# Performance work log

Measured on AMD Instinct MI355X. Metric: run time of the kernel, lower is better.

Reference implementation:

```python
import jax, jax.numpy as jnp
import numpy as np

B, S, D, H = 4, 1024, 1024, 16
HD = D // H


def setup_inputs() -> dict:
    key = jax.random.key(0)
    ks = jax.random.split(key, 8)
    x = jax.random.normal(ks[0], (B, S, D), dtype=jnp.float32)
    attn_bias = jax.random.normal(ks[1], (B, H, S, S), dtype=jnp.float32) * 0.1
    pos_ids = jnp.broadcast_to(jnp.arange(S, dtype=jnp.int32), (B, S))
    lengths = jnp.array([S, S - 64, S - 128, S - 256], dtype=jnp.int32)
    pad_mask = jnp.arange(S)[None, :] >= lengths[:, None]  # True = padded key
    scale = 0.02
    Wq = jax.random.normal(ks[2], (D, D), dtype=jnp.float32) * scale
    Wk = jax.random.normal(ks[3], (D, D), dtype=jnp.float32) * scale
    Wv = jax.random.normal(ks[4], (D, D), dtype=jnp.float32) * scale
    Wo = jax.random.normal(ks[5], (D, D), dtype=jnp.float32) * scale
    bq = jnp.zeros((D,), jnp.float32); bk = jnp.zeros((D,), jnp.float32)
    bv = jnp.zeros((D,), jnp.float32); bo = jnp.zeros((D,), jnp.float32)
    return {"x": x, "attn_bias": attn_bias, "pos_ids": pos_ids, "pad_mask": pad_mask,
            "Wq": Wq, "bq": bq, "Wk": Wk, "bk": bk, "Wv": Wv, "bv": bv, "Wo": Wo, "bo": bo}


def _apply_rotary(q, k, pos_ids):
    # q,k: [B,S,H,HD]; pos_ids: [B,S]
    hd = q.shape[-1]
    inv_freq = 1.0 / (10000.0 ** (jnp.arange(0, hd, 2, dtype=jnp.float32) / hd))
    freqs = pos_ids.astype(jnp.float32)[:, :, None] * inv_freq  # [B,S,HD/2]
    emb = jnp.concatenate([freqs, freqs], axis=-1)[:, :, None, :]  # [B,S,1,HD]
    cos, sin = jnp.cos(emb), jnp.sin(emb)
    def rot_half(t):
        t1, t2 = jnp.split(t, 2, axis=-1)
        return jnp.concatenate([-t2, t1], axis=-1)
    return q * cos + rot_half(q) * sin, k * cos + rot_half(k) * sin


def reference(x, attn_bias, pos_ids, pad_mask, Wq, bq, Wk, bk, Wv, bv, Wo, bo):
    b, s, d = x.shape
    q = (x @ Wq.T + bq).reshape(b, s, H, HD)
    k = (x @ Wk.T + bk).reshape(b, s, H, HD)
    v = (x @ Wv.T + bv).reshape(b, s, H, HD)
    q, k = _apply_rotary(q, k, pos_ids)
    q = q.transpose(0, 2, 1, 3)  # [B,H,S,HD]
    k = k.transpose(0, 2, 1, 3)
    v = v.transpose(0, 2, 1, 3)
    scores = jnp.einsum("bhqd,bhkd->bhqk", q, k) / np.sqrt(HD).astype(np.float32)
    scores = scores + attn_bias
    scores = jnp.where(pad_mask[:, None, None, :], -jnp.inf, scores)
    attn = jax.nn.softmax(scores, axis=-1)  # dropout p=0 -> identity
    out = jnp.einsum("bhqk,bhkd->bqhd", attn, v).reshape(b, s, d)
    metric = k.mean(axis=1)  # mean over heads -> [B,S,HD]
    return out @ Wo.T + bo, metric
```

## Files before the change

### kernel.cpp

```cpp
#include <hip/hip_runtime.h>
#include <hip/hip_bf16.h>

#define SS 1024
#define DD 1024
#define HH 16
#define HDD 64

using f32x4  = __attribute__((ext_vector_type(4))) float;
using bf16x8 = __attribute__((ext_vector_type(8))) __bf16;
using bf16x4 = __attribute__((ext_vector_type(4))) __bf16;

__device__ __forceinline__ void gload_lds16(const void* g, void* l) {
  __builtin_amdgcn_global_load_lds((__attribute__((address_space(1))) void*)g,
                                   (__attribute__((address_space(3))) void*)l, 16, 0, 0);
}

__global__ void convert_kernel(const float4* __restrict__ x, const float4* __restrict__ Wq,
                               const float4* __restrict__ Wk, const float4* __restrict__ Wv,
                               const float4* __restrict__ Wo,
                               bf16x4* __restrict__ xb, bf16x4* __restrict__ wqkvb,
                               bf16x4* __restrict__ wob, float4* __restrict__ metric) {
  int i = blockIdx.x * 256 + threadIdx.x;
  if (blockIdx.x < 256) {
    float4 z = {0.f, 0.f, 0.f, 0.f};
    metric[blockIdx.x * 256 + threadIdx.x] = z;
  }
  float4 v; bf16x4* dst;
  if (i < 1048576)      { v = x[i];              dst = xb + i; }
  else if (i < 1310720) { v = Wq[i - 1048576];   dst = wqkvb + (i - 1048576); }
  else if (i < 1572864) { v = Wk[i - 1310720];   dst = wqkvb + 262144 + (i - 1310720); }
  else if (i < 1835008) { v = Wv[i - 1572864];   dst = wqkvb + 524288 + (i - 1572864); }
  else                  { v = Wo[i - 1835008];   dst = wob + (i - 1835008); }
  bf16x4 o;
  o[0] = (__bf16)v.x; o[1] = (__bf16)v.y; o[2] = (__bf16)v.z; o[3] = (__bf16)v.w;
  *dst = o;
}

#define GEMM_STAGE(BUF, KK)                                                        \
  {                                                                                \
    char* Ab = smem + (BUF) * 32768;                                               \
    char* Bb = Ab + 16384;                                                         \
    _Pragma("unroll") for (int q = 0; q < 4; ++q) {                                \
      int idx = q * 256 + tid;                                                     \
      int row = idx >> 3, c = idx & 7;                                             \
      gload_lds16(A  + (size_t)(m0 + row) * 1024 + (KK) + ((c ^ (row & 7)) << 3),  \
                  Ab + q * 4096 + wid * 1024);                                     \
      gload_lds16(Bm + (size_t)(n0 + row) * 1024 + (KK) + ((c ^ (row & 7)) << 3),  \
                  Bb + q * 4096 + wid * 1024);                                     \
    }                                                                              \
  }

template<int EPI>
__global__ __launch_bounds__(256, 2)
void gemm_kernel(const __bf16* __restrict__ A, const __bf16* __restrict__ Bm, int N,
                 const float* __restrict__ b0, const float* __restrict__ b1,
                 const float* __restrict__ b2, const int* __restrict__ pos_ids,
                 __bf16* __restrict__ Qr, __bf16* __restrict__ Kr, __bf16* __restrict__ Vtg,
                 float* __restrict__ metric, float* __restrict__ Cout) {
  __shared__ __align__(16) char smem[65536];
  const int tid = threadIdx.x;
  const int wid = tid >> 6, lane = tid & 63;
  const int g = lane >> 4, cl = lane & 15;
  const int ntn = N >> 7;
  const int tile = (blockIdx.x & 7) * ((int)gridDim.x >> 3) + (blockIdx.x >> 3);
  const int bm = tile / ntn, bn = tile % ntn;
  const int m0 = bm << 7, n0 = bn << 7;
  const int wr = (wid >> 1) << 6, wc = (wid & 1) << 6;
  const int swz = cl & 7;

  f32x4 acc[4][4] = {};

  GEMM_STAGE(0, 0);
  __syncthreads();
  int buf = 0;
  for (int t = 0; t < 16; ++t) {
    if (t + 1 < 16) GEMM_STAGE(buf ^ 1, (t + 1) * 64);
    const __bf16* Abuf = (const __bf16*)(smem + buf * 32768);
    const __bf16* Bbuf = Abuf + 8192;
#pragma unroll
    for (int s = 0; s < 2; ++s) {
      bf16x8 fa[4], fb[4];
#pragma unroll
      for (int i = 0; i < 4; ++i)
        fa[i] = *(const bf16x8*)(Abuf + (wr + i * 16 + cl) * 64 + (((s * 4 + g) ^ swz) << 3));
#pragma unroll
      for (int j = 0; j < 4; ++j)
        fb[j] = *(const bf16x8*)(Bbuf + (wc + j * 16 + cl) * 64 + (((s * 4 + g) ^ swz) << 3));
#pragma unroll
      for (int i = 0; i < 4; ++i)
#pragma unroll
        for (int j = 0; j < 4; ++j)
          acc[i][j] = __builtin_amdgcn_mfma_f32_16x16x32_bf16(fa[i], fb[j], acc[i][j], 0, 0, 0);
    }
    __syncthreads();
    buf ^= 1;
  }

  if constexpr (EPI == 1) {
#pragma unroll
    for (int j = 0; j < 4; ++j) {
      int col = n0 + wc + j * 16 + cl;
      float bv = b0[col];
#pragma unroll
      for (int i = 0; i < 4; ++i)
#pragma unroll
        for (int r = 0; r < 4; ++r) {
          int row = m0 + wr + i * 16 + g * 4 + r;
          Cout[(size_t)row * 1024 + col] = acc[i][j][r] + bv;
        }
    }
  } else if (n0 >= 2048) {
    __bf16* vt_s = (__bf16*)smem;
    const int b_ = m0 >> 10, s0 = m0 & 1023;
    const int vbase = n0 - 2048;
#pragma unroll
    for (int phase = 0; phase < 2; ++phase) {
      __syncthreads();
      if ((wid & 1) == phase) {
#pragma unroll
        for (int j = 0; j < 4; ++j) {
          int d = j * 16 + cl;
          float bv = b2[vbase + wc + d];
#pragma unroll
          for (int i = 0; i < 4; ++i)
#pragma unroll
            for (int r = 0; r < 4; ++r)
              vt_s[d * 136 + wr + i * 16 + g * 4 + r] = (__bf16)(acc[i][j][r] + bv);
        }
      }
      __syncthreads();
      int hh = (vbase >> 6) + phase;
#pragma unroll
      for (int p = 0; p < 4; ++p) {
        int d = p * 16 + (tid >> 4), s8 = (tid & 15) * 8;
        bf16x8 v = *(const bf16x8*)(vt_s + d * 136 + s8);
        *(bf16x8*)(Vtg + ((size_t)(b_ * HH + hh) * HDD + d) * SS + s0 + s8) = v;
      }
    }
  } else {
    const int cb = n0 + wc;
    const int region = cb >> 10;
    const int hcol = (cb & 1023) >> 6;
    const int cir = cb & 1023;
    const float* bias = region == 0 ? b0 : b1;
    __bf16* dst = region == 0 ? Qr : Kr;
    float invf0 = exp2f(-0.4152410118609203f * (float)(cl));
    float invf1 = exp2f(-0.4152410118609203f * (float)(16 + cl));
#pragma unroll
    for (int i = 0; i < 4; ++i) {
#pragma unroll
      for (int r = 0; r < 4; ++r) {
        int row = m0 + wr + i * 16 + g * 4 + r;
        int b_ = row >> 10, s = row & 1023;
        size_t ob = ((size_t)(b_ * HH + hcol) * SS + s) * HDD;
        float pos = (float)pos_ids[row];
#pragma unroll
        for (int j = 0; j < 2; ++j) {
          int dlo = j * 16 + cl;
          float vlo = acc[i][j][r]     + bias[cir + dlo];
          float vhi = acc[i][j + 2][r] + bias[cir + dlo + 32];
          float th = pos * (j == 0 ? invf0 : invf1);
          float sn, cs;
          __sincosf(th, &sn, &cs);
          float olo = vlo * cs - vhi * sn;
          float ohi = vhi * cs + vlo * sn;
          dst[ob + dlo]      = (__bf16)olo;
          dst[ob + dlo + 32] = (__bf16)ohi;
          if (region == 1) {
            atomicAdd(&metric[(size_t)row * HDD + dlo],      olo * 0.0625f);
            atomicAdd(&metric[(size_t)row * HDD + dlo + 32], ohi * 0.0625f);
          }
        }
      }
    }
  }
}

#define ATTN_HALF(KT0, W0, BCUR)                                                   \
  {                                                                                \
    f32x4 sc[4];                                                                   \
    __builtin_amdgcn_s_setprio(1);                                                 \
    _Pragma("unroll") for (int kt = 0; kt < 4; ++kt) {                             \
      int row = (KT0 + kt) * 16 + cl;                                              \
      bf16x8 kb0 = *(const bf16x8*)(&Ks[buf][row][(g ^ swz) * 8]);                 \
      bf16x8 kb1 = *(const bf16x8*)(&Ks[buf][row][((g + 4) ^ swz) * 8]);           \
      f32x4 z = {0.f, 0.f, 0.f, 0.f};                                              \
      z = __builtin_amdgcn_mfma_f32_16x16x32_bf16(kb0, aq0, z, 0, 0, 0);           \
      sc[kt] = __builtin_amdgcn_mfma_f32_16x16x32_bf16(kb1, aq1, z, 0, 0, 0);      \
    }                                                                              \
    __builtin_amdgcn_s_setprio(0);                                                 \
    _Pragma("unroll") for (int kt = 0; kt < 4; ++kt)                               \
      _Pragma("unroll") for (int r = 0; r < 4; ++r)                                \
        sc[kt][r] = sc[kt][r] * 0.125f + BCUR[KT0 + kt][r];                        \
    float mx = fmaxf(fmaxf(fmaxf(sc[0][0], sc[0][1]), fmaxf(sc[0][2], sc[0][3])),  \
                     fmaxf(fmaxf(sc[1][0], sc[1][1]), fmaxf(sc[1][2], sc[1][3]))); \
    mx = fmaxf(mx, fmaxf(fmaxf(fmaxf(sc[2][0], sc[2][1]), fmaxf(sc[2][2], sc[2][3])), \
                         fmaxf(fmaxf(sc[3][0], sc[3][1]), fmaxf(sc[3][2], sc[3][3])))); \
    mx = fmaxf(mx, __shfl_xor(mx, 16, 64));                                        \
    mx = fmaxf(mx, __shfl_xor(mx, 32, 64));                                        \
    if (!__all(mx <= m_l + 8.0f)) {                                                \
      float nm = fmaxf(m_l, mx);                                                   \
      float s_ = __expf(m_l - nm);                                                 \
      m_l = nm; l_l *= s_;                                                         \
      float sb0 = __shfl(s_, 4 * g + 0, 64), sb1 = __shfl(s_, 4 * g + 1, 64);      \
      float sb2 = __shfl(s_, 4 * g + 2, 64), sb3 = __shfl(s_, 4 * g + 3, 64);      \
      _Pragma("unroll") for (int dj = 0; dj < 4; ++dj) {                           \
        o[dj][0] *= sb0; o[dj][1] *= sb1; o[dj][2] *= sb2; o[dj][3] *= sb3;        \
      }                                                                            \
    }                                                                              \
    _Pragma("unroll") for (int kt = 0; kt < 4; ++kt)                               \
      _Pragma("unroll") for (int r = 0; r < 4; ++r)                                \
        sc[kt][r] = __expf(sc[kt][r] - m_l);                                       \
    float rs = ((sc[0][0] + sc[0][1]) + (sc[0][2] + sc[0][3]))                     \
             + ((sc[1][0] + sc[1][1]) + (sc[1][2] + sc[1][3]))                     \
             + ((sc[2][0] + sc[2][1]) + (sc[2][2] + sc[2][3]))                     \
             + ((sc[3][0] + sc[3][1]) + (sc[3][2] + sc[3][3]));                    \
    rs += __shfl_xor(rs, 16, 64);                                                  \
    rs += __shfl_xor(rs, 32, 64);                                                  \
    l_l += rs;                                                                     \
    _Pragma("unroll") for (int w = 0; w < 2; ++w) {                                \
      _Pragma("unroll") for (int k2 = 0; k2 < 2; ++k2) {                           \
        int kt = w * 2 + k2;                                                       \
        bf16x4 pk;                                                                 \
        pk[0] = (__bf16)sc[kt][0]; pk[1] = (__bf16)sc[kt][1];                      \
        pk[2] = (__bf16)sc[kt][2]; pk[3] = (__bf16)sc[kt][3];                      \
        *(bf16x4*)(Pw + cl * 40 + k2 * 16 + 4 * g) = pk;                           \
      }                                                                            \
      bf16x8 pa = *(const bf16x8*)(Pw + cl * 40 + g * 8);                          \
      __builtin_amdgcn_s_setprio(1);                                               \
      _Pragma("unroll") for (int dj = 0; dj < 4; ++dj) {                           \
        int vrow = dj * 16 + cl;                                                   \
        bf16x8 vb = *(const bf16x8*)(&Vt[buf][vrow][((((W0 + w) * 4) + g) ^ swz) * 8]); \
        o[dj] = __builtin_amdgcn_mfma_f32_16x16x32_bf16(pa, vb, o[dj], 0, 0, 0);   \
      }                                                                            \
      __builtin_amdgcn_s_setprio(0);                                               \
    }                                                                              \
  }

#define ATTN_STAGE(NB, KK)                                                         \
  _Pragma("unroll") for (int s = 0; s < 2; ++s) {                                  \
    gload_lds16(Kb + (size_t)((KK) + s * 64 + krow) * 64 + kchk * 8,               \
                (char*)&Ks[NB][s * 64 + 8 * wid][0]);                              \
    gload_lds16(Vb + (size_t)(s * 32 + vrow) * SS + (KK) + vchk * 8,               \
                (char*)&Vt[NB][s * 32 + 4 * wid][0]);                              \
  }

__global__ __launch_bounds__(512, 4)
void attn_kernel(const __bf16* __restrict__ Qr, const __bf16* __restrict__ Kr,
                 const __bf16* __restrict__ Vtg, const float* __restrict__ bias,
                 const int* __restrict__ pad, __bf16* __restrict__ attn_out) {
  __shared__ __align__(16) __bf16 Ks[2][128][64];
  __shared__ __align__(16) __bf16 Vt[2][64][128];
  __shared__ __align__(16) __bf16 Plds[8][16][40];
  const int tid = threadIdx.x;
  const int wid = tid >> 6, lane = tid & 63;
  const int g = lane >> 4, cl = lane & 15;
  const int bh = blockIdx.x & 63, b_ = bh >> 4, h = bh & 15;
  const int q0 = (blockIdx.x >> 6) * 128 + wid * 16;
  const __bf16* Qb = Qr  + ((size_t)bh << 16);
  const __bf16* Kb = Kr  + ((size_t)bh << 16);
  const __bf16* Vb = Vtg + ((size_t)bh << 16);
  const float*  Bb = bias + ((size_t)bh << 20);
  const int* padb = pad + b_ * SS;

  int pm = (lane < 16) ? padb[lane * 64] : 1;
  unsigned long long ball = __ballot(pm == 0);
  const int valid64 = __popcll(ball & 0xFFFFull);
  const int nt = (valid64 + 1) >> 1;
  const int tail = valid64 & 1;

  const int krow = 8 * wid + (lane >> 3);
  const int kchk = (lane & 7) ^ (lane >> 3);
  const int vrow = 4 * wid + (lane >> 4);
  const int vchk = (lane & 15) ^ (vrow & 7);
  const int swz = cl & 7;
  __bf16* Pw = &Plds[wid][0][0];

  bf16x8 aq0 = *(const bf16x8*)(Qb + (size_t)(q0 + cl) * 64 + g * 8);
  bf16x8 aq1 = *(const bf16x8*)(Qb + (size_t)(q0 + cl) * 64 + 32 + g * 8);
  __builtin_amdgcn_sched_barrier(0);

  ATTN_STAGE(0, 0);
  __builtin_amdgcn_sched_barrier(0);
  f32x4 breg[8];
#pragma unroll
  for (int kt = 0; kt < 8; ++kt)
    breg[kt] = *(const f32x4*)(Bb + (size_t)(q0 + cl) * SS + kt * 16 + 4 * g);
  __builtin_amdgcn_sched_barrier(0);

  f32x4 o[4] = {};
  float m_l = -1e30f, l_l = 0.f;

  for (int t = 0; t < nt; ++t) {
    const int buf = t & 1;
    asm volatile("s_waitcnt vmcnt(8)" ::: "memory");
    __builtin_amdgcn_s_barrier();
    __builtin_amdgcn_sched_barrier(0);
    if (t + 1 < nt) {
      ATTN_STAGE(buf ^ 1, (t + 1) * 128);
      __builtin_amdgcn_sched_barrier(0);
    }

    ATTN_HALF(0, 0, breg);

    if (t + 1 < nt) {
      int kk2 = (t + 1) * 128;
#pragma unroll
      for (int kt = 0; kt < 4; ++kt)
        breg[kt] = *(const f32x4*)(Bb + (size_t)(q0 + cl) * SS + kk2 + kt * 16 + 4 * g);
      __builtin_amdgcn_sched_barrier(0);
    }

    if (!(tail && t == nt - 1))
      ATTN_HALF(4, 2, breg);

    if (t + 1 < nt) {
      int kk2 = (t + 1) * 128;
#pragma unroll
      for (int kt = 4; kt < 8; ++kt)
        breg[kt] = *(const f32x4*)(Bb + (size_t)(q0 + cl) * SS + kk2 + kt * 16 + 4 * g);
      __builtin_amdgcn_sched_barrier(0);
    }
  }

  float lb0 = __shfl(l_l, 4 * g + 0, 64), lb1 = __shfl(l_l, 4 * g + 1, 64);
  float lb2 = __shfl(l_l, 4 * g + 2, 64), lb3 = __shfl(l_l, 4 * g + 3, 64);
  float ib0 = 1.f / lb0, ib1 = 1.f / lb1, ib2 = 1.f / lb2, ib3 = 1.f / lb3;
#pragma unroll
  for (int dj = 0; dj < 4; ++dj) {
    int col = h * 64 + dj * 16 + cl;
    attn_out[(size_t)(b_ * SS + q0 + g * 4 + 0) * DD + col] = (__bf16)(o[dj][0] * ib0);
    attn_out[(size_t)(b_ * SS + q0 + g * 4 + 1) * DD + col] = (__bf16)(o[dj][1] * ib1);
    attn_out[(size_t)(b_ * SS + q0 + g * 4 + 2) * DD + col] = (__bf16)(o[dj][2] * ib2);
    attn_out[(size_t)(b_ * SS + q0 + g * 4 + 3) * DD + col] = (__bf16)(o[dj][3] * ib3);
  }
}

extern "C" void kernel_launch(void* const* d_in, const int* in_sizes, int n_in,
                              void* d_out, int out_size, void* d_ws, size_t ws_size,
                              hipStream_t stream) {
  const float* x  = (const float*)d_in[0];
  const float* ab = (const float*)d_in[1];
  const int* pos  = (const int*)d_in[2];
  const int* pad  = (const int*)d_in[3];
  const float* Wq = (const float*)d_in[4];
  const float* bq = (const float*)d_in[5];
  const float* Wk = (const float*)d_in[6];
  const float* bk = (const float*)d_in[7];
  const float* Wv = (const float*)d_in[8];
  const float* bv = (const float*)d_in[9];
  const float* Wo = (const float*)d_in[10];
  const float* bo = (const float*)d_in[11];
  float* out = (float*)d_out;
  float* metric = out + 4194304;

  char* ws = (char*)d_ws;
  __bf16* Qr   = (__bf16*)(ws);
  __bf16* Kr   = (__bf16*)(ws + 8388608);
  __bf16* Vtg  = (__bf16*)(ws + 16777216);
  __bf16* xb   = (__bf16*)(ws + 25165824);
  __bf16* wqkv = (__bf16*)(ws + 33554432);
  __bf16* wob  = (__bf16*)(ws + 39845888);
  __bf16* ao   = (__bf16*)(ws + 41943040);

  convert_kernel<<<8192, 256, 0, stream>>>((const float4*)x, (const float4*)Wq,
                                           (const float4*)Wk, (const float4*)Wv,
                                           (const float4*)Wo, (bf16x4*)xb,
                                           (bf16x4*)wqkv, (bf16x4*)wob, (float4*)metric);
  gemm_kernel<0><<<768, 256, 0, stream>>>(xb, wqkv, 3072, bq, bk, bv, pos,
                                          Qr, Kr, Vtg, metric, nullptr);
  attn_kernel<<<512, 512, 0, stream>>>(Qr, Kr, Vtg, ab, pad, ao);
  gemm_kernel<1><<<256, 256, 0, stream>>>(ao, wob, 1024, bo, nullptr, nullptr, nullptr,
                                          nullptr, nullptr, nullptr, nullptr, out);
}
```

Measured before the change: 155.3 us.

## Use 256x256 tiles with 8 waves for the QKV projection GEMM

The QKV projection GEMM moves from 128x128 tiles with 4 waves to 256x256 tiles with 8 waves, using 128KB of dynamic shared memory for double buffering. Prefetch loads are interleaved with the MFMA quarters, and priority and scheduling barriers are added. The larger tile is meant to raise arithmetic intensity and cut global and LDS traffic per FLOP. The cost is only 192 blocks on a GPU with 256 CUs, at one block per CU, so some CUs sit idle and there is less latency hiding. The output-projection GEMM is split out unchanged as its own kernel.

```diff
diff --git a/kernel.cpp b/kernel.cpp
--- a/kernel.cpp
+++ b/kernel.cpp
@@ -36,109 +36,120 @@
   *dst = o;
 }
 
-#define GEMM_STAGE(BUF, KK)                                                        \
-  {                                                                                \
-    char* Ab = smem + (BUF) * 32768;                                               \
-    char* Bb = Ab + 16384;                                                         \
-    _Pragma("unroll") for (int q = 0; q < 4; ++q) {                                \
-      int idx = q * 256 + tid;                                                     \
-      int row = idx >> 3, c = idx & 7;                                             \
-      gload_lds16(A  + (size_t)(m0 + row) * 1024 + (KK) + ((c ^ (row & 7)) << 3),  \
-                  Ab + q * 4096 + wid * 1024);                                     \
-      gload_lds16(Bm + (size_t)(n0 + row) * 1024 + (KK) + ((c ^ (row & 7)) << 3),  \
-                  Bb + q * 4096 + wid * 1024);                                     \
-    }                                                                              \
-  }
-
-template<int EPI>
-__global__ __launch_bounds__(256, 2)
-void gemm_kernel(const __bf16* __restrict__ A, const __bf16* __restrict__ Bm, int N,
+__global__ __launch_bounds__(512, 2)
+void gemm256_qkv(const __bf16* __restrict__ A, const __bf16* __restrict__ Bm,
                  const float* __restrict__ b0, const float* __restrict__ b1,
                  const float* __restrict__ b2, const int* __restrict__ pos_ids,
                  __bf16* __restrict__ Qr, __bf16* __restrict__ Kr, __bf16* __restrict__ Vtg,
-                 float* __restrict__ metric, float* __restrict__ Cout) {
-  __shared__ __align__(16) char smem[65536];
+                 float* __restrict__ metric) {
+  extern __shared__ __align__(16) char smem[];
   const int tid = threadIdx.x;
   const int wid = tid >> 6, lane = tid & 63;
   const int g = lane >> 4, cl = lane & 15;
-  const int ntn = N >> 7;
-  const int tile = (blockIdx.x & 7) * ((int)gridDim.x >> 3) + (blockIdx.x >> 3);
-  const int bm = tile / ntn, bn = tile % ntn;
-  const int m0 = bm << 7, n0 = bn << 7;
-  const int wr = (wid >> 1) << 6, wc = (wid & 1) << 6;
+  const int tile = (blockIdx.x & 7) * 24 + (blockIdx.x >> 3);
+  const int bm = tile / 12, bn = tile % 12;
+  const int m0 = bm << 8, n0 = bn << 8;
+  const int wm = wid >> 2, wn = wid & 3;
+  const int wr = wm << 7, wc = wn << 6;
   const int swz = cl & 7;
 
-  f32x4 acc[4][4] = {};
-
-  GEMM_STAGE(0, 0);
+  f32x4 acc[8][4] = {};
+
+  const int srow = tid >> 3, schk0 = tid & 7;
+
+#define G256_STAGE_ONE(DSTBASE, SRC, Q, KK)                                        \
+  {                                                                                \
+    int row_ = (Q) * 64 + srow;                                                    \
+    gload_lds16(SRC + (size_t)(row_) * 1024 + (KK) + ((schk0 ^ (row_ & 7)) << 3),  \
+                (char*)(DSTBASE) + (Q) * 8192 + wid * 1024);                       \
+  }
+
+  {
+    char* Ab = smem;  char* Bb = smem + 32768;
+#pragma unroll
+    for (int q = 0; q < 4; ++q) {
+      G256_STAGE_ONE(Ab, (A + (size_t)m0 * 1024), q, 0);
+      G256_STAGE_ONE(Bb, (Bm + (size_t)n0 * 1024), q, 0);
+    }
+  }
   __syncthreads();
-  int buf = 0;
+
   for (int t = 0; t < 16; ++t) {
-    if (t + 1 < 16) GEMM_STAGE(buf ^ 1, (t + 1) * 64);
-    const __bf16* Abuf = (const __bf16*)(smem + buf * 32768);
-    const __bf16* Bbuf = Abuf + 8192;
-#pragma unroll
-    for (int s = 0; s < 2; ++s) {
-      bf16x8 fa[4], fb[4];
+    const __bf16* As = (const __bf16*)(smem + (t & 1) * 65536);
+    const __bf16* Bs = As + 16384;
+    char* Adst = smem + ((t + 1) & 1) * 65536;
+    char* Bdst = Adst + 32768;
+    const int kk1 = (t + 1) * 64;
+    const bool pf = (t + 1 < 16);
+
+#pragma unroll
+    for (int p = 0; p < 4; ++p) {
+      if (pf) {
+        G256_STAGE_ONE(Adst, (A + (size_t)m0 * 1024), p, kk1);
+        G256_STAGE_ONE(Bdst, (Bm + (size_t)n0 * 1024), p, kk1);
+      }
+      const int qm = p & 1, qn = p >> 1;
+      bf16x8 fa0[4], fa1[4], fb0[2], fb1[2];
+#pragma unroll
+      for (int i = 0; i < 4; ++i) {
+        const __bf16* rp = As + (size_t)(wr + qm * 64 + i * 16 + cl) * 64;
+        fa0[i] = *(const bf16x8*)(rp + ((g ^ swz) << 3));
+        fa1[i] = *(const bf16x8*)(rp + (((4 + g) ^ swz) << 3));
+      }
+#pragma unroll
+      for (int j = 0; j < 2; ++j) {
+        const __bf16* rp = Bs + (size_t)(wc + qn * 32 + j * 16 + cl) * 64;
+        fb0[j] = *(const bf16x8*)(rp + ((g ^ swz) << 3));
+        fb1[j] = *(const bf16x8*)(rp + (((4 + g) ^ swz) << 3));
+      }
+      __builtin_amdgcn_s_setprio(1);
 #pragma unroll
       for (int i = 0; i < 4; ++i)
-        fa[i] = *(const bf16x8*)(Abuf + (wr + i * 16 + cl) * 64 + (((s * 4 + g) ^ swz) << 3));
-#pragma unroll
-      for (int j = 0; j < 4; ++j)
-        fb[j] = *(const bf16x8*)(Bbuf + (wc + j * 16 + cl) * 64 + (((s * 4 + g) ^ swz) << 3));
-#pragma unroll
-      for (int i = 0; i < 4; ++i)
-#pragma unroll
-        for (int j = 0; j < 4; ++j)
-          acc[i][j] = __builtin_amdgcn_mfma_f32_16x16x32_bf16(fa[i], fb[j], acc[i][j], 0, 0, 0);
+#pragma unroll
+        for (int j = 0; j < 2; ++j) {
+          acc[qm * 4 + i][qn * 2 + j] = __builtin_amdgcn_mfma_f32_16x16x32_bf16(
+              fa0[i], fb0[j], acc[qm * 4 + i][qn * 2 + j], 0, 0, 0);
+          acc[qm * 4 + i][qn * 2 + j] = __builtin_amdgcn_mfma_f32_16x16x32_bf16(
+              fa1[i], fb1[j], acc[qm * 4 + i][qn * 2 + j], 0, 0, 0);
+        }
+      __builtin_amdgcn_s_setprio(0);
+      __builtin_amdgcn_sched_barrier(0);
     }
     __syncthreads();
-    buf ^= 1;
-  }
-
-  if constexpr (EPI == 1) {
-#pragma unroll
-    for (int j = 0; j < 4; ++j) {
-      int col = n0 + wc + j * 16 + cl;
-      float bv = b0[col];
-#pragma unroll
-      for (int i = 0; i < 4; ++i)
-#pragma unroll
-        for (int r = 0; r < 4; ++r) {
-          int row = m0 + wr + i * 16 + g * 4 + r;
-          Cout[(size_t)row * 1024 + col] = acc[i][j][r] + bv;
-        }
-    }
-  } else if (n0 >= 2048) {
+  }
+
+  const int cb = n0 + wc;
+  if (cb >= 2048) {
     __bf16* vt_s = (__bf16*)smem;
     const int b_ = m0 >> 10, s0 = m0 & 1023;
     const int vbase = n0 - 2048;
-#pragma unroll
-    for (int phase = 0; phase < 2; ++phase) {
-      __syncthreads();
-      if ((wid & 1) == phase) {
+    __syncthreads();
+#pragma unroll
+    for (int hl = 0; hl < 4; ++hl) {
+      if (wn == hl) {
 #pragma unroll
         for (int j = 0; j < 4; ++j) {
           int d = j * 16 + cl;
-          float bv = b2[vbase + wc + d];
-#pragma unroll
-          for (int i = 0; i < 4; ++i)
+          float bv = b2[vbase + hl * 64 + d];
+#pragma unroll
+          for (int i = 0; i < 8; ++i)
 #pragma unroll
             for (int r = 0; r < 4; ++r)
-              vt_s[d * 136 + wr + i * 16 + g * 4 + r] = (__bf16)(acc[i][j][r] + bv);
+              vt_s[d * 264 + wr + i * 16 + g * 4 + r] = (__bf16)(acc[i][j][r] + bv);
         }
       }
       __syncthreads();
-      int hh = (vbase >> 6) + phase;
+      int hh = (vbase >> 6) + hl;
 #pragma unroll
       for (int p = 0; p < 4; ++p) {
-        int d = p * 16 + (tid >> 4), s8 = (tid & 15) * 8;
-        bf16x8 v = *(const bf16x8*)(vt_s + d * 136 + s8);
+        int idx = p * 512 + tid;
+        int d = idx >> 5, s8 = (idx & 31) * 8;
+        bf16x8 v = *(const bf16x8*)(vt_s + d * 264 + s8);
         *(bf16x8*)(Vtg + ((size_t)(b_ * HH + hh) * HDD + d) * SS + s0 + s8) = v;
       }
+      __syncthreads();
     }
   } else {
-    const int cb = n0 + wc;
     const int region = cb >> 10;
     const int hcol = (cb & 1023) >> 6;
     const int cir = cb & 1023;
@@ -147,7 +158,7 @@
     float invf0 = exp2f(-0.4152410118609203f * (float)(cl));
     float invf1 = exp2f(-0.4152410118609203f * (float)(16 + cl));
 #pragma unroll
-    for (int i = 0; i < 4; ++i) {
+    for (int i = 0; i < 8; ++i) {
 #pragma unroll
       for (int r = 0; r < 4; ++r) {
         int row = m0 + wr + i * 16 + g * 4 + r;
@@ -173,6 +184,75 @@
         }
       }
     }
+  }
+}
+
+#define GEMM_STAGE(BUF, KK)                                                        \
+  {                                                                                \
+    char* Ab = smem + (BUF) * 32768;                                               \
+    char* Bb = Ab + 16384;                                                         \
+    _Pragma("unroll") for (int q = 0; q < 4; ++q) {                                \
+      int idx = q * 256 + tid;                                                     \
+      int row = idx >> 3, c = idx & 7;                                             \
+      gload_lds16(A  + (size_t)(m0 + row) * 1024 + (KK) + ((c ^ (row & 7)) << 3),  \
+                  Ab + q * 4096 + wid * 1024);                                     \
+      gload_lds16(Bm + (size_t)(n0 + row) * 1024 + (KK) + ((c ^ (row & 7)) << 3),  \
+                  Bb + q * 4096 + wid * 1024);                                     \
+    }                                                                              \
+  }
+
+__global__ __launch_bounds__(256, 2)
+void gemm_oproj(const __bf16* __restrict__ A, const __bf16* __restrict__ Bm,
+                const float* __restrict__ b0, float* __restrict__ Cout) {
+  __shared__ __align__(16) char smem[65536];
+  const int tid = threadIdx.x;
+  const int wid = tid >> 6, lane = tid & 63;
+  const int g = lane >> 4, cl = lane & 15;
+  const int tile = (blockIdx.x & 7) * ((int)gridDim.x >> 3) + (blockIdx.x >> 3);
+  const int bm = tile >> 3, bn = tile & 7;
+  const int m0 = bm << 7, n0 = bn << 7;
+  const int wr = (wid >> 1) << 6, wc = (wid & 1) << 6;
+  const int swz = cl & 7;
+
+  f32x4 acc[4][4] = {};
+
+  GEMM_STAGE(0, 0);
+  __syncthreads();
+  int buf = 0;
+  for (int t = 0; t < 16; ++t) {
+    if (t + 1 < 16) GEMM_STAGE(buf ^ 1, (t + 1) * 64);
+    const __bf16* Abuf = (const __bf16*)(smem + buf * 32768);
+    const __bf16* Bbuf = Abuf + 8192;
+#pragma unroll
+    for (int s = 0; s < 2; ++s) {
+      bf16x8 fa[4], fb[4];
+#pragma unroll
+      for (int i = 0; i < 4; ++i)
+        fa[i] = *(const bf16x8*)(Abuf + (wr + i * 16 + cl) * 64 + (((s * 4 + g) ^ swz) << 3));
+#pragma unroll
+      for (int j = 0; j < 4; ++j)
+        fb[j] = *(const bf16x8*)(Bbuf + (wc + j * 16 + cl) * 64 + (((s * 4 + g) ^ swz) << 3));
+#pragma unroll
+      for (int i = 0; i < 4; ++i)
+#pragma unroll
+        for (int j = 0; j < 4; ++j)
+          acc[i][j] = __builtin_amdgcn_mfma_f32_16x16x32_bf16(fa[i], fb[j], acc[i][j], 0, 0, 0);
+    }
+    __syncthreads();
+    buf ^= 1;
+  }
+
+#pragma unroll
+  for (int j = 0; j < 4; ++j) {
+    int col = n0 + wc + j * 16 + cl;
+    float bv = b0[col];
+#pragma unroll
+    for (int i = 0; i < 4; ++i)
+#pragma unroll
+      for (int r = 0; r < 4; ++r) {
+        int row = m0 + wr + i * 16 + g * 4 + r;
+        Cout[(size_t)row * 1024 + col] = acc[i][j][r] + bv;
+      }
   }
 }
 
@@ -363,13 +443,15 @@
   __bf16* wob  = (__bf16*)(ws + 39845888);
   __bf16* ao   = (__bf16*)(ws + 41943040);
 
+  hipFuncSetAttribute((const void*)gemm256_qkv,
+                      hipFuncAttributeMaxDynamicSharedMemorySize, 131072);
+
   convert_kernel<<<8192, 256, 0, stream>>>((const float4*)x, (const float4*)Wq,
                                            (const float4*)Wk, (const float4*)Wv,
                                            (const float4*)Wo, (bf16x4*)xb,
                                            (bf16x4*)wqkv, (bf16x4*)wob, (float4*)metric);
-  gemm_kernel<0><<<768, 256, 0, stream>>>(xb, wqkv, 3072, bq, bk, bv, pos,
-                                          Qr, Kr, Vtg, metric, nullptr);
+  gemm256_qkv<<<192, 512, 131072, stream>>>(xb, wqkv, bq, bk, bv, pos,
+                                            Qr, Kr, Vtg, metric);
   attn_kernel<<<512, 512, 0, stream>>>(Qr, Kr, Vtg, ab, pad, ao);
-  gemm_kernel<1><<<256, 256, 0, stream>>>(ao, wob, 1024, bo, nullptr, nullptr, nullptr,
-                                          nullptr, nullptr, nullptr, nullptr, out);
-}
+  gemm_oproj<<<256, 256, 0, stream>>>(ao, wob, bo, out);
+}
```

After: 158.7 us. 2.2% more time.

## Compute head-mean metric via averaged K weights instead of atomics

Applied to the files above, without the earlier changes.

Uses linearity (rotary is identical across heads) to precompute the head-averaged K weight rows and bias in a new prep kernel. These are appended as an extra 128-wide N tile to the QKV GEMM, whose epilogue writes the metric directly. This removes the metric zeroing and the per-element atomicAdds in the K epilogue. The cost is one extra small kernel and 32 more GEMM tiles, which are half-wasted since only the first 64 columns are used. Precision also changes because averaged weights are rounded to bf16.

```diff
diff --git a/kernel.cpp b/kernel.cpp
--- a/kernel.cpp
+++ b/kernel.cpp
@@ -19,12 +19,8 @@
                                const float4* __restrict__ Wk, const float4* __restrict__ Wv,
                                const float4* __restrict__ Wo,
                                bf16x4* __restrict__ xb, bf16x4* __restrict__ wqkvb,
-                               bf16x4* __restrict__ wob, float4* __restrict__ metric) {
+                               bf16x4* __restrict__ wob) {
   int i = blockIdx.x * 256 + threadIdx.x;
-  if (blockIdx.x < 256) {
-    float4 z = {0.f, 0.f, 0.f, 0.f};
-    metric[blockIdx.x * 256 + threadIdx.x] = z;
-  }
   float4 v; bf16x4* dst;
   if (i < 1048576)      { v = x[i];              dst = xb + i; }
   else if (i < 1310720) { v = Wq[i - 1048576];   dst = wqkvb + (i - 1048576); }
@@ -34,6 +30,29 @@
   bf16x4 o;
   o[0] = (__bf16)v.x; o[1] = (__bf16)v.y; o[2] = (__bf16)v.z; o[3] = (__bf16)v.w;
   *dst = o;
+}
+
+__global__ void prep_kernel(const __bf16* __restrict__ wqkv, const float* __restrict__ bk,
+                            __bf16* __restrict__ wkavg, float* __restrict__ bkavg) {
+  int idx = blockIdx.x * 512 + threadIdx.x;
+  int d = idx >> 7, k8 = (idx & 127) * 8;
+  float s[8] = {};
+#pragma unroll
+  for (int h = 0; h < 16; ++h) {
+    bf16x8 v = *(const bf16x8*)(wqkv + (size_t)(1024 + h * 64 + d) * 1024 + k8);
+#pragma unroll
+    for (int j = 0; j < 8; ++j) s[j] += (float)v[j];
+  }
+  bf16x8 o;
+#pragma unroll
+  for (int j = 0; j < 8; ++j) o[j] = (__bf16)(s[j] * 0.0625f);
+  *(bf16x8*)(wkavg + (size_t)d * 1024 + k8) = o;
+  if (blockIdx.x == 0 && threadIdx.x < 64) {
+    float b = 0.f;
+#pragma unroll
+    for (int h = 0; h < 16; ++h) b += bk[h * 64 + threadIdx.x];
+    bkavg[threadIdx.x] = b * 0.0625f;
+  }
 }
 
 #define GEMM_STAGE(BUF, KK)                                                        \
@@ -54,7 +73,8 @@
 __global__ __launch_bounds__(256, 2)
 void gemm_kernel(const __bf16* __restrict__ A, const __bf16* __restrict__ Bm, int N,
                  const float* __restrict__ b0, const float* __restrict__ b1,
-                 const float* __restrict__ b2, const int* __restrict__ pos_ids,
+                 const float* __restrict__ b2, const float* __restrict__ bavg,
+                 const int* __restrict__ pos_ids,
                  __bf16* __restrict__ Qr, __bf16* __restrict__ Kr, __bf16* __restrict__ Vtg,
                  float* __restrict__ metric, float* __restrict__ Cout) {
   __shared__ __align__(16) char smem[65536];
@@ -109,6 +129,30 @@
           Cout[(size_t)row * 1024 + col] = acc[i][j][r] + bv;
         }
     }
+  } else if (n0 >= 3072) {
+    if (wc == 0) {
+      float invf0 = exp2f(-0.4152410118609203f * (float)(cl));
+      float invf1 = exp2f(-0.4152410118609203f * (float)(16 + cl));
+#pragma unroll
+      for (int i = 0; i < 4; ++i) {
+#pragma unroll
+        for (int r = 0; r < 4; ++r) {
+          int row = m0 + wr + i * 16 + g * 4 + r;
+          float pos = (float)pos_ids[row];
+#pragma unroll
+          for (int j = 0; j < 2; ++j) {
+            int dlo = j * 16 + cl;
+            float vlo = acc[i][j][r]     + bavg[dlo];
+            float vhi = acc[i][j + 2][r] + bavg[dlo + 32];
+            float th = pos * (j == 0 ? invf0 : invf1);
+            float sn, cs;
+            __sincosf(th, &sn, &cs);
+            metric[(size_t)row * HDD + dlo]      = vlo * cs - vhi * sn;
+            metric[(size_t)row * HDD + dlo + 32] = vhi * cs + vlo * sn;
+          }
+        }
+      }
+    }
   } else if (n0 >= 2048) {
     __bf16* vt_s = (__bf16*)smem;
     const int b_ = m0 >> 10, s0 = m0 & 1023;
@@ -166,10 +210,6 @@
           float ohi = vhi * cs + vlo * sn;
           dst[ob + dlo]      = (__bf16)olo;
           dst[ob + dlo + 32] = (__bf16)ohi;
-          if (region == 1) {
-            atomicAdd(&metric[(size_t)row * HDD + dlo],      olo * 0.0625f);
-            atomicAdd(&metric[(size_t)row * HDD + dlo + 32], ohi * 0.0625f);
-          }
         }
       }
     }
@@ -355,21 +395,23 @@
   float* metric = out + 4194304;
 
   char* ws = (char*)d_ws;
-  __bf16* Qr   = (__bf16*)(ws);
-  __bf16* Kr   = (__bf16*)(ws + 8388608);
-  __bf16* Vtg  = (__bf16*)(ws + 16777216);
-  __bf16* xb   = (__bf16*)(ws + 25165824);
-  __bf16* wqkv = (__bf16*)(ws + 33554432);
-  __bf16* wob  = (__bf16*)(ws + 39845888);
-  __bf16* ao   = (__bf16*)(ws + 41943040);
+  __bf16* Qr    = (__bf16*)(ws);
+  __bf16* Kr    = (__bf16*)(ws + 8388608);
+  __bf16* Vtg   = (__bf16*)(ws + 16777216);
+  __bf16* xb    = (__bf16*)(ws + 25165824);
+  __bf16* wqkv  = (__bf16*)(ws + 33554432);
+  __bf16* wob   = (__bf16*)(ws + 40108032);
+  __bf16* ao    = (__bf16*)(ws + 42205184);
+  float*  bkavg = (float*)(ws + 50593792);
 
   convert_kernel<<<8192, 256, 0, stream>>>((const float4*)x, (const float4*)Wq,
                                            (const float4*)Wk, (const float4*)Wv,
                                            (const float4*)Wo, (bf16x4*)xb,
-                                           (bf16x4*)wqkv, (bf16x4*)wob, (float4*)metric);
-  gemm_kernel<0><<<768, 256, 0, stream>>>(xb, wqkv, 3072, bq, bk, bv, pos,
+                                           (bf16x4*)wqkv, (bf16x4*)wob);
+  prep_kernel<<<16, 512, 0, stream>>>(wqkv, bk, wqkv + (size_t)3072 * 1024, bkavg);
+  gemm_kernel<0><<<800, 256, 0, stream>>>(xb, wqkv, 3200, bq, bk, bv, bkavg, pos,
                                           Qr, Kr, Vtg, metric, nullptr);
   attn_kernel<<<512, 512, 0, stream>>>(Qr, Kr, Vtg, ab, pad, ao);
   gemm_kernel<1><<<256, 256, 0, stream>>>(ao, wob, 1024, bo, nullptr, nullptr, nullptr,
-                                          nullptr, nullptr, nullptr, nullptr, out);
-}
+                                          nullptr, nullptr, nullptr, nullptr, nullptr, out);
+}
```

Measured after the change: 143.7 us, median of 2. 7.5% less time.
